# Kernel optimization log

Hardware: AMD Instinct MI355X
Metric: run time of the kernel (lower is better)

The kernel has to match this reference:

```python
import jax, jax.numpy as jnp
import numpy as np

EMB = 1024
NUM_HEADS = 16
KEY_SIZE = 64
HEAD_SIZE = 64
EPS = 1.1920929e-07  # torch RMSNorm default eps=None -> finfo(float32).eps


def setup_inputs() -> dict:
    key = jax.random.key(0)
    ks = jax.random.split(key, 6)
    B, S = 2, 2048
    qkv_out = 2 * KEY_SIZE * NUM_HEADS + HEAD_SIZE * NUM_HEADS  # 3072
    return {
        "embeddings": jax.random.normal(ks[0], (B, S, EMB), dtype=jnp.float32),
        "cos_buffer": jax.random.uniform(ks[1], (S, KEY_SIZE), dtype=jnp.float32),
        "sin_buffer": jax.random.uniform(ks[2], (S, KEY_SIZE), dtype=jnp.float32),
        "norm_weight": jnp.ones((EMB,), dtype=jnp.float32),
        "qkv_weight": jax.random.normal(ks[3], (qkv_out, EMB), dtype=jnp.float32) * (EMB ** -0.5),
        "out_weight": jax.random.normal(ks[4], (EMB, NUM_HEADS * HEAD_SIZE), dtype=jnp.float32) * ((NUM_HEADS * HEAD_SIZE) ** -0.5),
    }


def _rotate(feat, cos_b, sin_b):
    # feat: [B, H, S, key_size]; torch code: cat(second_half, first_half) (no negation)
    half = KEY_SIZE // 2
    swapped = jnp.concatenate((feat[..., half:], feat[..., :half]), axis=-1)
    return cos_b * feat + sin_b * swapped


def reference(embeddings, cos_buffer, sin_buffer, norm_weight, qkv_weight, out_weight):
    B, S, D = embeddings.shape
    # RMSNorm
    rms = jnp.sqrt(jnp.mean(embeddings * embeddings, axis=-1, keepdims=True) + EPS)
    normed = embeddings / rms * norm_weight
    # fused QKV projection (torch Linear: x @ W.T)
    qkv = normed @ qkv_weight.T  # [B, S, 3072]
    ks = KEY_SIZE * NUM_HEADS
    q = qkv[..., :ks].reshape(B, S, NUM_HEADS, KEY_SIZE).transpose(0, 2, 1, 3)
    k = qkv[..., ks:2 * ks].reshape(B, S, NUM_HEADS, KEY_SIZE).transpose(0, 2, 1, 3)
    v = qkv[..., 2 * ks:].reshape(B, S, NUM_HEADS, HEAD_SIZE).transpose(0, 2, 1, 3)
    q = _rotate(q, cos_buffer, sin_buffer)
    k = _rotate(k, cos_buffer, sin_buffer)
    # causal scaled dot product attention
    scale = 1.0 / jnp.sqrt(jnp.float32(KEY_SIZE))
    scores = jnp.einsum("bhqd,bhkd->bhqk", q, k) * scale  # [B,H,S,S]
    causal = jnp.tril(jnp.ones((S, S), dtype=bool))
    scores = jnp.where(causal, scores, jnp.float32(-jnp.inf))
    probs = jax.nn.softmax(scores, axis=-1)
    attn = jnp.einsum("bhqk,bhkd->bhqd", probs, v)  # [B,H,S,head]
    attn = attn.transpose(0, 2, 1, 3).reshape(B, S, NUM_HEADS * HEAD_SIZE)
    out = attn @ out_weight.T
    return embeddings + out
```

## Files before the change

### kernel.cpp

```cpp
#include <hip/hip_runtime.h>
#include <hip/hip_bf16.h>
#include <stdint.h>

#define EMB 1024
#define SEQ 2048
#define NB 2
#define NH 16
#define HD 64
#define QKVN 3072
#define BSROWS (NB*SEQ)

typedef __attribute__((ext_vector_type(8))) short short8;
typedef __attribute__((ext_vector_type(4))) float f32x4;
typedef __attribute__((ext_vector_type(4))) unsigned short u16x4;

__device__ __forceinline__ float bf2f(unsigned short u){
  union{uint32_t i; float f;} x; x.i = ((uint32_t)u)<<16; return x.f;
}
__device__ __forceinline__ unsigned short f2bf(float f){
  union{float f; uint32_t i;} x; x.f = f;
  return (unsigned short)((x.i + 0x7FFFu + ((x.i>>16)&1u))>>16);
}

__device__ __forceinline__ void gload_lds16(const void* g, void* l){
  __builtin_amdgcn_global_load_lds((const __attribute__((address_space(1))) void*)g,
                                   (__attribute__((address_space(3))) void*)l, 16, 0, 0);
}

__global__ __launch_bounds__(256) void k_rmsnorm(const float* __restrict__ x,
                                                 const float* __restrict__ w,
                                                 unsigned short* __restrict__ out){
  int row = blockIdx.x;
  const float4* xr = (const float4*)(x + (size_t)row*EMB);
  float4 v = xr[threadIdx.x];
  float ss = v.x*v.x + v.y*v.y + v.z*v.z + v.w*v.w;
  #pragma unroll
  for(int m=1;m<64;m<<=1) ss += __shfl_xor(ss, m, 64);
  __shared__ float red[4];
  if((threadIdx.x & 63)==0) red[threadIdx.x>>6] = ss;
  __syncthreads();
  float tot = red[0]+red[1]+red[2]+red[3];
  float rinv = rsqrtf(tot*(1.0f/EMB) + 1.1920929e-07f);
  float4 wv = ((const float4*)w)[threadIdx.x];
  u16x4 o;
  o.x = f2bf(v.x*wv.x*rinv); o.y = f2bf(v.y*wv.y*rinv);
  o.z = f2bf(v.z*wv.z*rinv); o.w = f2bf(v.w*wv.w*rinv);
  *(u16x4*)(out + (size_t)row*EMB + threadIdx.x*4) = o;
}

__global__ __launch_bounds__(256) void k_f2bf(const float* __restrict__ in,
                                              unsigned short* __restrict__ out, int n4){
  int i = blockIdx.x*256 + threadIdx.x;
  if(i < n4){
    float4 v = ((const float4*)in)[i];
    u16x4 o;
    o.x = f2bf(v.x); o.y = f2bf(v.y); o.z = f2bf(v.z); o.w = f2bf(v.w);
    ((u16x4*)out)[i] = o;
  }
}

template<int MODE>
__global__ __launch_bounds__(256) void k_gemm(const unsigned short* __restrict__ A,
                                              const unsigned short* __restrict__ W,
                                              unsigned short* __restrict__ Cb,
                                              float* __restrict__ Cf,
                                              const float* __restrict__ resid,
                                              int M, int N, int K){
  __shared__ unsigned short As[128*32];
  __shared__ unsigned short Bs[128*32];
  const int tid = threadIdx.x;
  const int l  = tid & 63;
  const int wid = tid >> 6;
  const int lr = l & 15, lh = l >> 4;
  const int m0 = blockIdx.y * 128, n0 = blockIdx.x * 128;
  const int wr = wid >> 1, wc = wid & 1;

  f32x4 acc[4][4] = {};

  const int nk = K >> 5;
  for(int kt=0; kt<nk; kt++){
    const int k0 = kt*32;
    #pragma unroll
    for(int j=0;j<2;j++){
      int c = j*256 + tid;
      int r = c >> 2, kc = (c & 3)*8;
      gload_lds16(A + (size_t)(m0+r)*K + k0 + kc, &As[(size_t)(j*256 + wid*64)*8]);
      gload_lds16(W + (size_t)(n0+r)*K + k0 + kc, &Bs[(size_t)(j*256 + wid*64)*8]);
    }
    __syncthreads();
    short8 af[4], bfr[4];
    #pragma unroll
    for(int i=0;i<4;i++){
      af[i]  = *(const short8*)&As[(size_t)((wr*64 + i*16 + lr)*32 + lh*8)];
      bfr[i] = *(const short8*)&Bs[(size_t)((wc*64 + i*16 + lr)*32 + lh*8)];
    }
    #pragma unroll
    for(int i=0;i<4;i++)
      #pragma unroll
      for(int jn=0;jn<4;jn++)
        acc[i][jn] = __builtin_amdgcn_mfma_f32_16x16x32_bf16(af[i], bfr[jn], acc[i][jn], 0,0,0);
    __syncthreads();
  }

  const int rbase = m0 + wr*64, cbase = n0 + wc*64;
  #pragma unroll
  for(int i=0;i<4;i++){
    #pragma unroll
    for(int jn=0;jn<4;jn++){
      int rr = rbase + i*16 + lh*4;
      int cc = cbase + jn*16 + lr;
      #pragma unroll
      for(int t=0;t<4;t++){
        float val = acc[i][jn][t];
        if(MODE==0){
          Cb[(size_t)(rr+t)*N + cc] = f2bf(val);
        } else {
          Cf[(size_t)(rr+t)*N + cc] = val + resid[(size_t)(rr+t)*N + cc];
        }
      }
    }
  }
}

__global__ __launch_bounds__(256) void k_rope(const unsigned short* __restrict__ qkv,
                                              const float* __restrict__ cosb,
                                              const float* __restrict__ sinb,
                                              unsigned short* __restrict__ qb,
                                              unsigned short* __restrict__ kb){
  int t = blockIdx.x*256 + threadIdx.x;
  int g = t & 7;
  int h = (t >> 3) & 15;
  int part = (t >> 7) & 1;
  int r = t >> 8;
  int b = r >> 11, s = r & 2047;
  const unsigned short* src = qkv + (size_t)r*QKVN + part*1024 + h*64 + g*4;
  u16x4 xl = *(const u16x4*)src;
  u16x4 xh = *(const u16x4*)(src + 32);
  f32x4 cl = *(const f32x4*)(cosb + s*64 + g*4);
  f32x4 ch = *(const f32x4*)(cosb + s*64 + 32 + g*4);
  f32x4 sl = *(const f32x4*)(sinb + s*64 + g*4);
  f32x4 sh = *(const f32x4*)(sinb + s*64 + 32 + g*4);
  u16x4 lo, hi;
  #pragma unroll
  for(int j=0;j<4;j++){
    float a = bf2f(xl[j]), bb = bf2f(xh[j]);
    lo[j] = f2bf(cl[j]*a  + sl[j]*bb);
    hi[j] = f2bf(ch[j]*bb + sh[j]*a);
  }
  unsigned short* dst = (part ? kb : qb) + ((size_t)((b*NH + h)*SEQ + s))*HD + g*4;
  *(u16x4*)dst = lo;
  *(u16x4*)(dst + 32) = hi;
}

__global__ __launch_bounds__(256) void k_vt(const unsigned short* __restrict__ qkv,
                                            unsigned short* __restrict__ vt){
  __shared__ unsigned short t[64][65];
  int bh = blockIdx.y;
  int b = bh >> 4, h = bh & 15;
  int s0 = blockIdx.x*64;
  int tid = threadIdx.x;
  #pragma unroll
  for(int it=0; it<4; it++){
    int idx = it*256 + tid;
    int si = idx >> 4;
    int dj = (idx & 15)*4;
    const unsigned short* g = qkv + (size_t)(b*SEQ + s0 + si)*QKVN + 2048 + h*64 + dj;
    u16x4 v = *(const u16x4*)g;
    t[dj+0][si] = v.x; t[dj+1][si] = v.y; t[dj+2][si] = v.z; t[dj+3][si] = v.w;
  }
  __syncthreads();
  int d = tid >> 2, sc = (tid & 3)*16;
  unsigned short* out = vt + (size_t)(bh*64 + d)*SEQ + s0 + sc;
  #pragma unroll
  for(int u=0;u<4;u++){
    u16x4 o;
    #pragma unroll
    for(int e=0;e<4;e++){
      int n = sc + u*4 + e;
      int blk32 = n >> 5, n32 = n & 31;
      int nc = n32 >> 2, e4 = n32 & 3;
      int oc = (nc & 1) ? (4 + (nc >> 1)) : (nc >> 1);
      o[e] = t[d][blk32*32 + oc*4 + e4];
    }
    *(u16x4*)(out + u*4) = o;
  }
}

__global__ __launch_bounds__(256, 4) void k_attn(const unsigned short* __restrict__ Q,
                                                 const unsigned short* __restrict__ K,
                                                 const unsigned short* __restrict__ Vt,
                                                 unsigned short* __restrict__ O){
  __shared__ unsigned short Ks[2][64*64];
  __shared__ unsigned short Vs[2][64*64];
  const int tid = threadIdx.x;
  const int l = tid & 63, wid = tid >> 6;
  const int lr = l & 15, lh = l >> 4;
  const int id = blockIdx.x;
  const int slot = id >> 3;
  const int bh  = (id & 7)*4 + (slot & 3);
  const int qblk = 31 - (slot >> 2);
  const int q0 = qblk*64 + wid*16;
  const unsigned short* Qp = Q + ((size_t)bh*SEQ + q0)*HD;
  const unsigned short* Kp = K + (size_t)bh*SEQ*HD;
  const unsigned short* Vp = Vt + (size_t)bh*HD*SEQ;

  short8 qf0 = *(const short8*)&Qp[lr*HD + lh*8];
  short8 qf1 = *(const short8*)&Qp[lr*HD + 32 + lh*8];

  f32x4 o[4] = {};
  float m_ = -__builtin_inff();
  float ls = 0.f;
  const float scale = 0.125f;
  const int qg = q0 + lr;
  const int swz = lr & 7;
  const int T = qblk + 1;

  #define STAGE(t_, b_) { \
    const int kv0s = (t_)*64; \
    _Pragma("unroll") \
    for(int j=0;j<2;j++){ \
      int s = j*256 + tid; \
      int sb = j*256 + wid*64; \
      int r = s >> 3, c = s & 7; \
      gload_lds16(Kp + (size_t)(kv0s + r)*HD + ((c ^ (r & 7))*8), &Ks[b_][sb*8]); \
      gload_lds16(Vp + (size_t)r*SEQ + kv0s + ((c ^ (r & 7))*8), &Vs[b_][sb*8]); \
    } }

  STAGE(0, 0);
  __syncthreads();
  int cur = 0;

  for(int t = 0; t < T; t++){
    const int kv0 = t*64;
    if(t + 1 < T) STAGE(t+1, cur^1);

    const unsigned short* Kb = Ks[cur];
    const unsigned short* Vb = Vs[cur];

    f32x4 s4[4] = {};
    #pragma unroll
    for(int i=0;i<4;i++){
      int row = i*16 + lr;
      short8 ka = *(const short8*)&Kb[(row*8 + (lh ^ swz))*8];
      short8 kc = *(const short8*)&Kb[(row*8 + ((4+lh) ^ swz))*8];
      s4[i] = __builtin_amdgcn_mfma_f32_16x16x32_bf16(ka, qf0, s4[i], 0,0,0);
      s4[i] = __builtin_amdgcn_mfma_f32_16x16x32_bf16(kc, qf1, s4[i], 0,0,0);
    }

    float v[16];
    #pragma unroll
    for(int i=0;i<4;i++)
      #pragma unroll
      for(int j=0;j<4;j++){
        int kvg = kv0 + i*16 + lh*4 + j;
        v[i*4+j] = (kvg <= qg) ? s4[i][j]*scale : -__builtin_inff();
      }
    float mx = v[0];
    #pragma unroll
    for(int j=1;j<16;j++) mx = fmaxf(mx, v[j]);
    mx = fmaxf(mx, __shfl_xor(mx, 16, 64));
    mx = fmaxf(mx, __shfl_xor(mx, 32, 64));
    float mn = fmaxf(m_, mx);
    float cr = __expf(m_ - mn);
    float p[16], rs = 0.f;
    #pragma unroll
    for(int j=0;j<16;j++){ p[j] = __expf(v[j] - mn); rs += p[j]; }
    rs += __shfl_xor(rs, 16, 64);
    rs += __shfl_xor(rs, 32, 64);
    ls = ls*cr + rs;
    m_ = mn;

    short8 pb0, pb1;
    #pragma unroll
    for(int j=0;j<8;j++){ pb0[j] = (short)f2bf(p[j]); pb1[j] = (short)f2bf(p[8+j]); }

    #pragma unroll
    for(int f=0; f<4; f++) o[f] *= cr;
    #pragma unroll
    for(int f=0; f<4; f++){
      int row = f*16 + lr;
      short8 va = *(const short8*)&Vb[(row*8 + (lh ^ swz))*8];
      short8 vb2 = *(const short8*)&Vb[(row*8 + ((4+lh) ^ swz))*8];
      o[f] = __builtin_amdgcn_mfma_f32_16x16x32_bf16(va, pb0, o[f], 0,0,0);
      o[f] = __builtin_amdgcn_mfma_f32_16x16x32_bf16(vb2, pb1, o[f], 0,0,0);
    }

    __syncthreads();
    cur ^= 1;
  }
  #undef STAGE

  const int b = bh >> 4, h = bh & 15;
  const float inv = 1.0f/ls;
  #pragma unroll
  for(int f=0; f<4; f++){
    u16x4 ov;
    #pragma unroll
    for(int t2=0;t2<4;t2++) ov[t2] = f2bf(o[f][t2]*inv);
    *(u16x4*)&O[(size_t)(b*SEQ + qg)*EMB + h*HD + f*16 + lh*4] = ov;
  }
}

extern "C" void kernel_launch(void* const* d_in, const int* in_sizes, int n_in,
                              void* d_out, int out_size, void* d_ws, size_t ws_size,
                              hipStream_t stream) {
  const float* emb   = (const float*)d_in[0];
  const float* cosb  = (const float*)d_in[1];
  const float* sinb  = (const float*)d_in[2];
  const float* nw    = (const float*)d_in[3];
  const float* qkvw  = (const float*)d_in[4];
  const float* outw  = (const float*)d_in[5];
  float* out = (float*)d_out;

  unsigned short* ws = (unsigned short*)d_ws;
  unsigned short* qkvWb = ws;
  unsigned short* outWb = qkvWb + (size_t)QKVN*EMB;
  unsigned short* normed = outWb + (size_t)EMB*EMB;
  unsigned short* attnout = normed;
  unsigned short* qkvb = normed + (size_t)BSROWS*EMB;
  unsigned short* qb = qkvb + (size_t)BSROWS*QKVN;
  unsigned short* kb = qb + (size_t)NB*NH*SEQ*HD;
  unsigned short* vtb = kb + (size_t)NB*NH*SEQ*HD;

  k_rmsnorm<<<dim3(BSROWS), dim3(256), 0, stream>>>(emb, nw, normed);
  k_f2bf<<<dim3((QKVN*EMB/4 + 255)/256), dim3(256), 0, stream>>>(qkvw, qkvWb, QKVN*EMB/4);
  k_f2bf<<<dim3((EMB*EMB/4 + 255)/256), dim3(256), 0, stream>>>(outw, outWb, EMB*EMB/4);
  k_gemm<0><<<dim3(QKVN/128, BSROWS/128), dim3(256), 0, stream>>>(
      normed, qkvWb, qkvb, nullptr, nullptr, BSROWS, QKVN, EMB);
  k_rope<<<dim3(BSROWS, 1), dim3(256), 0, stream>>>(qkvb, cosb, sinb, qb, kb);
  k_vt<<<dim3(SEQ/64, NB*NH), dim3(256), 0, stream>>>(qkvb, vtb);
  k_attn<<<dim3(SEQ/64 * NB*NH), dim3(256), 0, stream>>>(qb, kb, vtb, attnout);
  k_gemm<1><<<dim3(EMB/128, BSROWS/128), dim3(256), 0, stream>>>(
      attnout, outWb, nullptr, out, emb, BSROWS, EMB, EMB);
}
```

Before: 208.5 us.

## Fold softmax scale into RoPE, peel causal tile, lazy rescale, merge weight casts

The softmax scale and log2(e) are folded into Q during RoPE, so attention can use exp2 directly and skip a per-score multiply. The causal mask now applies only to the final diagonal tile, which is peeled out of the main loop. The running max is rescaled lazily, only when a new max exceeds the old one by a threshold, and the row-sum shuffles are deferred to the end. Probabilities are packed with v_cvt_pk_bf16_f32, and the two weight-cast kernels are merged into one launch. Lazy rescaling lets exponentials grow up to about 2^11.5 before renormalizing, which could slightly affect accuracy.

```diff
diff --git a/kernel.cpp b/kernel.cpp
--- a/kernel.cpp
+++ b/kernel.cpp
@@ -48,15 +48,19 @@
   *(u16x4*)(out + (size_t)row*EMB + threadIdx.x*4) = o;
 }
 
-__global__ __launch_bounds__(256) void k_f2bf(const float* __restrict__ in,
-                                              unsigned short* __restrict__ out, int n4){
+__global__ __launch_bounds__(256) void k_f2bf2(const float* __restrict__ a,
+                                               const float* __restrict__ b,
+                                               unsigned short* __restrict__ oa,
+                                               unsigned short* __restrict__ ob,
+                                               int na4, int nb4){
   int i = blockIdx.x*256 + threadIdx.x;
-  if(i < n4){
-    float4 v = ((const float4*)in)[i];
-    u16x4 o;
-    o.x = f2bf(v.x); o.y = f2bf(v.y); o.z = f2bf(v.z); o.w = f2bf(v.w);
-    ((u16x4*)out)[i] = o;
-  }
+  const float* src; unsigned short* dst; int idx;
+  if(i < na4){ src = a; dst = oa; idx = i; }
+  else { idx = i - na4; if(idx >= nb4) return; src = b; dst = ob; }
+  float4 v = ((const float4*)src)[idx];
+  u16x4 o;
+  o.x = f2bf(v.x); o.y = f2bf(v.y); o.z = f2bf(v.z); o.w = f2bf(v.w);
+  ((u16x4*)dst)[idx] = o;
 }
 
 template<int MODE>
@@ -133,6 +137,7 @@
   int part = (t >> 7) & 1;
   int r = t >> 8;
   int b = r >> 11, s = r & 2047;
+  const float qs = part ? 1.0f : 0.125f*1.4426950408889634f;
   const unsigned short* src = qkv + (size_t)r*QKVN + part*1024 + h*64 + g*4;
   u16x4 xl = *(const u16x4*)src;
   u16x4 xh = *(const u16x4*)(src + 32);
@@ -144,8 +149,8 @@
   #pragma unroll
   for(int j=0;j<4;j++){
     float a = bf2f(xl[j]), bb = bf2f(xh[j]);
-    lo[j] = f2bf(cl[j]*a  + sl[j]*bb);
-    hi[j] = f2bf(ch[j]*bb + sh[j]*a);
+    lo[j] = f2bf((cl[j]*a  + sl[j]*bb)*qs);
+    hi[j] = f2bf((ch[j]*bb + sh[j]*a)*qs);
   }
   unsigned short* dst = (part ? kb : qb) + ((size_t)((b*NH + h)*SEQ + s))*HD + g*4;
   *(u16x4*)dst = lo;
@@ -210,7 +215,6 @@
   f32x4 o[4] = {};
   float m_ = -__builtin_inff();
   float ls = 0.f;
-  const float scale = 0.125f;
   const int qg = q0 + lr;
   const int swz = lr & 7;
   const int T = qblk + 1;
@@ -226,17 +230,8 @@
       gload_lds16(Vp + (size_t)r*SEQ + kv0s + ((c ^ (r & 7))*8), &Vs[b_][sb*8]); \
     } }
 
-  STAGE(0, 0);
-  __syncthreads();
-  int cur = 0;
-
-  for(int t = 0; t < T; t++){
-    const int kv0 = t*64;
-    if(t + 1 < T) STAGE(t+1, cur^1);
-
-    const unsigned short* Kb = Ks[cur];
-    const unsigned short* Vb = Vs[cur];
-
+  auto body = [&](int kv0, const unsigned short* Kb, const unsigned short* Vb,
+                  bool masked){
     f32x4 s4[4] = {};
     #pragma unroll
     for(int i=0;i<4;i++){
@@ -246,49 +241,67 @@
       s4[i] = __builtin_amdgcn_mfma_f32_16x16x32_bf16(ka, qf0, s4[i], 0,0,0);
       s4[i] = __builtin_amdgcn_mfma_f32_16x16x32_bf16(kc, qf1, s4[i], 0,0,0);
     }
-
     float v[16];
     #pragma unroll
     for(int i=0;i<4;i++)
       #pragma unroll
       for(int j=0;j<4;j++){
-        int kvg = kv0 + i*16 + lh*4 + j;
-        v[i*4+j] = (kvg <= qg) ? s4[i][j]*scale : -__builtin_inff();
+        float val = s4[i][j];
+        if(masked){
+          int kvg = kv0 + i*16 + lh*4 + j;
+          val = (kvg <= qg) ? val : -__builtin_inff();
+        }
+        v[i*4+j] = val;
       }
-    float mx = v[0];
-    #pragma unroll
-    for(int j=1;j<16;j++) mx = fmaxf(mx, v[j]);
-    mx = fmaxf(mx, __shfl_xor(mx, 16, 64));
-    mx = fmaxf(mx, __shfl_xor(mx, 32, 64));
-    float mn = fmaxf(m_, mx);
-    float cr = __expf(m_ - mn);
+    float pm = v[0];
+    #pragma unroll
+    for(int j=1;j<16;j++) pm = fmaxf(pm, v[j]);
+    if(__any(pm > m_ + 11.544f)){
+      float mx = fmaxf(pm, __shfl_xor(pm, 16, 64));
+      mx = fmaxf(mx, __shfl_xor(mx, 32, 64));
+      float mn = fmaxf(m_, mx);
+      float cr = __builtin_amdgcn_exp2f(m_ - mn);
+      m_ = mn;
+      ls *= cr;
+      #pragma unroll
+      for(int f=0; f<4; f++) o[f] *= cr;
+    }
     float p[16], rs = 0.f;
     #pragma unroll
-    for(int j=0;j<16;j++){ p[j] = __expf(v[j] - mn); rs += p[j]; }
-    rs += __shfl_xor(rs, 16, 64);
-    rs += __shfl_xor(rs, 32, 64);
-    ls = ls*cr + rs;
-    m_ = mn;
-
-    short8 pb0, pb1;
-    #pragma unroll
-    for(int j=0;j<8;j++){ pb0[j] = (short)f2bf(p[j]); pb1[j] = (short)f2bf(p[8+j]); }
-
-    #pragma unroll
-    for(int f=0; f<4; f++) o[f] *= cr;
+    for(int j=0;j<16;j++){ p[j] = __builtin_amdgcn_exp2f(v[j] - m_); rs += p[j]; }
+    ls += rs;
+
+    union { short8 s8; uint32_t u[4]; } P0, P1;
+    #pragma unroll
+    for(int j=0;j<4;j++){
+      asm("v_cvt_pk_bf16_f32 %0, %1, %2" : "=v"(P0.u[j]) : "v"(p[2*j]),   "v"(p[2*j+1]));
+      asm("v_cvt_pk_bf16_f32 %0, %1, %2" : "=v"(P1.u[j]) : "v"(p[8+2*j]), "v"(p[8+2*j+1]));
+    }
     #pragma unroll
     for(int f=0; f<4; f++){
       int row = f*16 + lr;
-      short8 va = *(const short8*)&Vb[(row*8 + (lh ^ swz))*8];
+      short8 va  = *(const short8*)&Vb[(row*8 + (lh ^ swz))*8];
       short8 vb2 = *(const short8*)&Vb[(row*8 + ((4+lh) ^ swz))*8];
-      o[f] = __builtin_amdgcn_mfma_f32_16x16x32_bf16(va, pb0, o[f], 0,0,0);
-      o[f] = __builtin_amdgcn_mfma_f32_16x16x32_bf16(vb2, pb1, o[f], 0,0,0);
-    }
-
+      o[f] = __builtin_amdgcn_mfma_f32_16x16x32_bf16(va,  P0.s8, o[f], 0,0,0);
+      o[f] = __builtin_amdgcn_mfma_f32_16x16x32_bf16(vb2, P1.s8, o[f], 0,0,0);
+    }
+  };
+
+  STAGE(0, 0);
+  __syncthreads();
+  int cur = 0;
+
+  for(int t = 0; t < T-1; t++){
+    STAGE(t+1, cur^1);
+    body(t*64, Ks[cur], Vs[cur], false);
     __syncthreads();
     cur ^= 1;
   }
+  body((T-1)*64, Ks[cur], Vs[cur], true);
   #undef STAGE
+
+  ls += __shfl_xor(ls, 16, 64);
+  ls += __shfl_xor(ls, 32, 64);
 
   const int b = bh >> 4, h = bh & 15;
   const float inv = 1.0f/ls;
@@ -322,9 +335,9 @@
   unsigned short* kb = qb + (size_t)NB*NH*SEQ*HD;
   unsigned short* vtb = kb + (size_t)NB*NH*SEQ*HD;
 
+  const int na4 = QKVN*EMB/4, nb4 = EMB*EMB/4;
   k_rmsnorm<<<dim3(BSROWS), dim3(256), 0, stream>>>(emb, nw, normed);
-  k_f2bf<<<dim3((QKVN*EMB/4 + 255)/256), dim3(256), 0, stream>>>(qkvw, qkvWb, QKVN*EMB/4);
-  k_f2bf<<<dim3((EMB*EMB/4 + 255)/256), dim3(256), 0, stream>>>(outw, outWb, EMB*EMB/4);
+  k_f2bf2<<<dim3((na4+nb4+255)/256), dim3(256), 0, stream>>>(qkvw, outw, qkvWb, outWb, na4, nb4);
   k_gemm<0><<<dim3(QKVN/128, BSROWS/128), dim3(256), 0, stream>>>(
       normed, qkvWb, qkvb, nullptr, nullptr, BSROWS, QKVN, EMB);
   k_rope<<<dim3(BSROWS, 1), dim3(256), 0, stream>>>(qkvb, cosb, sinb, qb, kb);
```

After: 198.0 us. 5.0% less time.
